# Kernel optimization log

Measured on AMD Instinct MI355X. Metric: run time of the kernel, lower is better.

The kernel has to match this reference:

```python
import jax, jax.numpy as jnp
import numpy as np

EMBED = 768
FFN = 3072
HEADS = 12
HEAD_DIM = EMBED // HEADS
B, T = 4, 2048


def _layer_norm(x, g, b, eps=1e-5):
    m = jnp.mean(x, axis=-1, keepdims=True)
    v = jnp.mean((x - m) ** 2, axis=-1, keepdims=True)
    return (x - m) * jax.lax.rsqrt(v + eps) * g + b


def setup_inputs() -> dict:
    key = jax.random.key(0)
    ks = jax.random.split(key, 8)
    s_e = 1.0 / np.sqrt(EMBED)
    s_f = 1.0 / np.sqrt(FFN)
    # weights stored [in, out] (transpose of torch Linear layout)
    return {
        "x": jax.random.normal(ks[0], (B, T, EMBED), dtype=jnp.float32),
        "ln1_g": jnp.ones((EMBED,), jnp.float32),
        "ln1_b": jnp.zeros((EMBED,), jnp.float32),
        "wq": jax.random.uniform(ks[1], (EMBED, EMBED), jnp.float32, -s_e, s_e),
        "bq": jnp.zeros((EMBED,), jnp.float32),
        "wk": jax.random.uniform(ks[2], (EMBED, EMBED), jnp.float32, -s_e, s_e),
        "bk": jnp.zeros((EMBED,), jnp.float32),
        "wv": jax.random.uniform(ks[3], (EMBED, EMBED), jnp.float32, -s_e, s_e),
        "bv": jnp.zeros((EMBED,), jnp.float32),
        "wo": jax.random.uniform(ks[4], (EMBED, EMBED), jnp.float32, -s_e, s_e),
        "bo": jnp.zeros((EMBED,), jnp.float32),
        "ln2_g": jnp.ones((EMBED,), jnp.float32),
        "ln2_b": jnp.zeros((EMBED,), jnp.float32),
        "w1": jax.random.uniform(ks[5], (EMBED, FFN), jnp.float32, -s_e, s_e),
        "b1": jnp.zeros((FFN,), jnp.float32),
        "w2": jax.random.uniform(ks[6], (FFN, EMBED), jnp.float32, -s_f, s_f),
        "b2": jnp.zeros((EMBED,), jnp.float32),
    }


def reference(x, ln1_g, ln1_b, wq, bq, wk, bk, wv, bv, wo, bo,
              ln2_g, ln2_b, w1, b1, w2, b2):
    Bx, Tx, C = x.shape
    # --- self-attention block (pre-norm) ---
    residual = x
    h = _layer_norm(x, ln1_g, ln1_b)
    q = (h @ wq + bq).reshape(Bx, Tx, HEADS, HEAD_DIM)
    k = (h @ wk + bk).reshape(Bx, Tx, HEADS, HEAD_DIM)
    v = (h @ wv + bv).reshape(Bx, Tx, HEADS, HEAD_DIM)
    scale = 1.0 / np.sqrt(HEAD_DIM)
    attn = jnp.einsum('bqhd,bkhd->bhqk', q, k) * scale  # [B,H,T,T]
    attn = jax.nn.softmax(attn, axis=-1)
    o = jnp.einsum('bhqk,bkhd->bqhd', attn, v).reshape(Bx, Tx, C)
    x = residual + (o @ wo + bo)
    # --- FFN block (pre-norm) ---
    residual = x
    h = _layer_norm(x, ln2_g, ln2_b)
    h = jax.nn.gelu(h @ w1 + b1, approximate=False)
    x = residual + (h @ w2 + b2)
    return x
```

## Files before the change

kernel.cpp:

```cpp
#include <hip/hip_runtime.h>
#include <hip/hip_bf16.h>

#define EMBED 768
#define FFNDIM 3072
#define HEADS 12
#define HDIM  64
#define BB    4
#define TT    2048
#define MTOK  (BB*TT)

typedef __hip_bfloat16 bf16;
typedef __attribute__((ext_vector_type(8))) short short8;
typedef __attribute__((ext_vector_type(4))) float f32x4;
typedef __attribute__((ext_vector_type(16))) float f32x16;
typedef __attribute__((ext_vector_type(4))) unsigned short ushort4v;

__device__ __forceinline__ f32x4 mfma16(short8 a, short8 b, f32x4 c) {
  return __builtin_amdgcn_mfma_f32_16x16x32_bf16(a, b, c, 0, 0, 0);
}
__device__ __forceinline__ f32x16 mfma32(short8 a, short8 b, f32x16 c) {
  return __builtin_amdgcn_mfma_f32_32x32x16_bf16(a, b, c, 0, 0, 0);
}

__device__ __forceinline__ unsigned short f2bf(float f) {
  union { float f; unsigned int u; } v; v.f = f;
  unsigned int u = v.u;
  return (unsigned short)((u + 0x7fffu + ((u >> 16) & 1u)) >> 16);
}

__device__ __forceinline__ unsigned cvtpk(float lo, float hi) {
  unsigned r;
  asm("v_cvt_pk_bf16_f32 %0, %1, %2" : "=v"(r) : "v"(lo), "v"(hi));
  return r;
}
__device__ __forceinline__ void pl32swap(unsigned& vdst, unsigned& vsrc) {
  asm("v_permlane32_swap_b32 %0, %1" : "+v"(vdst), "+v"(vsrc));
}

__device__ __forceinline__ void gl_lds16(const void* g, void* l) {
  __builtin_amdgcn_global_load_lds((const __attribute__((address_space(1))) void*)g,
                                   (__attribute__((address_space(3))) void*)l, 16, 0, 0);
}

struct TArgs {
  const float* src[6];
  bf16* dst[6];
  int K[6];
  int N[6];
};

__global__ __launch_bounds__(256) void transpose_k(TArgs ta) {
  const int mi = blockIdx.z;
  const int K = ta.K[mi], N = ta.N[mi];
  const int nt = N / 32;
  const int bx = blockIdx.x % nt, by = blockIdx.x / nt;
  const int n0 = bx * 32, k0 = by * 32;
  if (k0 >= K) return;
  __shared__ float t[32][33];
  const float* __restrict__ W = ta.src[mi];
  bf16* __restrict__ Wt = ta.dst[mi];
  const int tx = threadIdx.x & 31, ty = threadIdx.x >> 5;
#pragma unroll
  for (int i = 0; i < 4; ++i) {
    int kk = ty + i * 8;
    t[tx][kk] = W[(size_t)(k0 + kk) * N + n0 + tx];
  }
  __syncthreads();
#pragma unroll
  for (int i = 0; i < 4; ++i) {
    int nn = ty + i * 8;
    Wt[(size_t)(n0 + nn) * K + k0 + tx] = __float2bfloat16(t[nn][tx]);
  }
}

__global__ __launch_bounds__(256) void ln_k(const float* __restrict__ x,
                                            const float* __restrict__ g,
                                            const float* __restrict__ b,
                                            bf16* __restrict__ out) {
  const int row = blockIdx.x * 4 + (threadIdx.x >> 6);
  const int lane = threadIdx.x & 63;
  const float* xr = x + (size_t)row * EMBED;
  float4 v[3];
  float s = 0.f;
#pragma unroll
  for (int i = 0; i < 3; ++i) {
    v[i] = *(const float4*)&xr[i * 256 + lane * 4];
    s += v[i].x + v[i].y + v[i].z + v[i].w;
  }
#pragma unroll
  for (int m = 1; m < 64; m <<= 1) s += __shfl_xor(s, m);
  const float mean = s * (1.f / 768.f);
  float ss = 0.f;
#pragma unroll
  for (int i = 0; i < 3; ++i) {
    float dx = v[i].x - mean, dy = v[i].y - mean, dz = v[i].z - mean, dw = v[i].w - mean;
    ss += dx * dx + dy * dy + dz * dz + dw * dw;
  }
#pragma unroll
  for (int m = 1; m < 64; m <<= 1) ss += __shfl_xor(ss, m);
  const float rstd = rsqrtf(ss * (1.f / 768.f) + 1e-5f);
#pragma unroll
  for (int i = 0; i < 3; ++i) {
    float4 g4 = *(const float4*)&g[i * 256 + lane * 4];
    float4 b4 = *(const float4*)&b[i * 256 + lane * 4];
    ushort4v o4;
    o4[0] = f2bf((v[i].x - mean) * rstd * g4.x + b4.x);
    o4[1] = f2bf((v[i].y - mean) * rstd * g4.y + b4.y);
    o4[2] = f2bf((v[i].z - mean) * rstd * g4.z + b4.z);
    o4[3] = f2bf((v[i].w - mean) * rstd * g4.w + b4.w);
    *(ushort4v*)&out[(size_t)row * EMBED + i * 256 + lane * 4] = o4;
  }
}

template <int EPI>
__global__ __launch_bounds__(256) void gemm_bt_k(
    const bf16* __restrict__ A, const bf16* __restrict__ Bt,
    const float* __restrict__ bias, const float* __restrict__ bias2,
    const float* __restrict__ bias3, const float* __restrict__ resid,
    float* __restrict__ outf, bf16* __restrict__ outb,
    bf16* __restrict__ outk, bf16* __restrict__ outvt,
    int N, int K) {
  const int tid = threadIdx.x;
  const int lane = tid & 63;
  const int w = tid >> 6;
  const int wr = w >> 1, wc = w & 1;
  const int l16 = lane & 15, g = lane >> 4;

  const int nbx = N >> 7;
  const int logical = ((int)blockIdx.x & 7) * ((int)gridDim.x >> 3) + ((int)blockIdx.x >> 3);
  const int m0 = (logical / nbx) * 128, n0 = (logical % nbx) * 128;

  __shared__ bf16 Al[2][128 * 32];
  __shared__ bf16 Bl[2][128 * 32];

  f32x4 acc[4][4];
#pragma unroll
  for (int i = 0; i < 4; ++i)
#pragma unroll
    for (int j = 0; j < 4; ++j) acc[i][j] = {0.f, 0.f, 0.f, 0.f};

  const int st_r = lane >> 2;
  const int st_c = ((lane & 3) ^ ((lane >> 3) & 3)) * 8;
  const size_t a_base = (size_t)(m0 + w * 32) * K;
  const size_t b_base = (size_t)(n0 + w * 32) * K;

  auto stage = [&](int bufi, int kt) {
#pragma unroll
    for (int p = 0; p < 2; ++p) {
      gl_lds16(A + a_base + (size_t)(p * 16 + st_r) * K + kt + st_c,
               &Al[bufi][(w * 32 + p * 16) * 32]);
      gl_lds16(Bt + b_base + (size_t)(p * 16 + st_r) * K + kt + st_c,
               &Bl[bufi][(w * 32 + p * 16) * 32]);
    }
  };

  stage(0, 0);
  __syncthreads();
  int buf = 0;
  const int nt = K >> 5;
  const int sw = (l16 >> 1) & 3;
  for (int t = 0; t < nt; ++t) {
    if (t + 1 < nt) stage(buf ^ 1, (t + 1) * 32);
    short8 af[4], bfr[4];
#pragma unroll
    for (int i = 0; i < 4; ++i)
      af[i] = *(const short8*)&Al[buf][(wr * 64 + i * 16 + l16) * 32 + (g ^ sw) * 8];
#pragma unroll
    for (int j = 0; j < 4; ++j)
      bfr[j] = *(const short8*)&Bl[buf][(wc * 64 + j * 16 + l16) * 32 + (g ^ sw) * 8];
#pragma unroll
    for (int i = 0; i < 4; ++i)
#pragma unroll
      for (int j = 0; j < 4; ++j) acc[i][j] = mfma16(af[i], bfr[j], acc[i][j]);
    __syncthreads();
    buf ^= 1;
  }

  const int crow = m0 + wr * 64 + g * 4;
  const int ccol = n0 + wc * 64 + l16;

  if constexpr (EPI == 0) {
    const int region = n0 / EMBED;
    const float* bp = (region == 0) ? bias : (region == 1) ? bias2 : bias3;
    if (region < 2) {
      const float sc = (region == 0) ? 0.125f : 1.0f;
      bf16* __restrict__ dst = (region == 0) ? outb : outk;
#pragma unroll
      for (int j = 0; j < 4; ++j) {
        const int cn = ccol - region * EMBED + j * 16;
        const float bvv = bp[cn];
#pragma unroll
        for (int i = 0; i < 4; ++i)
#pragma unroll
          for (int rr = 0; rr < 4; ++rr) {
            const int m = crow + i * 16 + rr;
            dst[(size_t)m * EMBED + cn] = __float2bfloat16((acc[i][j][rr] + bvv) * sc);
          }
      }
    } else {
#pragma unroll
      for (int j = 0; j < 4; ++j) {
        const int cn = ccol - 2 * EMBED + j * 16;
        const float bvv = bp[cn];
        const int hh = cn >> 6, dd = cn & 63;
#pragma unroll
        for (int i = 0; i < 4; ++i) {
          const int m = crow + i * 16;
          const int bb2 = m >> 11, t = m & 2047;
          ushort4v pk;
#pragma unroll
          for (int rr = 0; rr < 4; ++rr) pk[rr] = f2bf(acc[i][j][rr] + bvv);
          *(ushort4v*)&outvt[((size_t)((bb2 * HEADS + hh) * HDIM + dd)) * TT + t] = pk;
        }
      }
    }
  } else if constexpr (EPI == 1) {
#pragma unroll
    for (int j = 0; j < 4; ++j) {
      const int cn = ccol + j * 16;
      const float bvv = bias[cn];
#pragma unroll
      for (int i = 0; i < 4; ++i)
#pragma unroll
        for (int rr = 0; rr < 4; ++rr) {
          const int m = crow + i * 16 + rr;
          const size_t idx = (size_t)m * N + cn;
          outf[idx] = resid[idx] + acc[i][j][rr] + bvv;
        }
    }
  } else {
#pragma unroll
    for (int j = 0; j < 4; ++j) {
      const int cn = ccol + j * 16;
      const float bvv = bias[cn];
#pragma unroll
      for (int i = 0; i < 4; ++i)
#pragma unroll
        for (int rr = 0; rr < 4; ++rr) {
          const int m = crow + i * 16 + rr;
          const float v = acc[i][j][rr] + bvv;
          const float ge = 0.5f * v * (1.f + erff(v * 0.70710678118f));
          outb[(size_t)m * N + cn] = __float2bfloat16(ge);
        }
    }
  }
}

__global__ __launch_bounds__(256) void flash4_k(const bf16* __restrict__ q,
                                                const bf16* __restrict__ k,
                                                const bf16* __restrict__ vt,
                                                bf16* __restrict__ o) {
  const int tid = threadIdx.x, lane = tid & 63;
  const int l32 = lane & 31, hl = lane >> 5;
  const int w = tid >> 6;
  const int logical = ((int)blockIdx.x & 7) * 96 + ((int)blockIdx.x >> 3);
  const int qt = logical & 15;
  const int hb = logical >> 4;
  const int h = hb % HEADS, b = hb / HEADS;
  const int q0 = (qt * 4 + w) * 32;

  __shared__ bf16 Kl[2][64 * 64];
  __shared__ bf16 Vl[2][64 * 64];

  short8 qf[4];
  {
    const bf16* qp = q + (size_t)(b * TT + q0 + l32) * EMBED + h * HDIM + hl * 8;
#pragma unroll
    for (int c = 0; c < 4; ++c) qf[c] = *(const short8*)&qp[c * 16];
  }

  const bf16* __restrict__ kgs = k + (size_t)(b * TT) * EMBED + h * HDIM;
  const bf16* __restrict__ vgs = vt + ((size_t)((b * HEADS + h) * HDIM)) * TT;

  f32x16 oacc0, oacc1;
#pragma unroll
  for (int i = 0; i < 16; ++i) { oacc0[i] = 0.f; oacc1[i] = 0.f; }
  float mrun = -1.0e30f, lrun = 0.f;

  const int st_rw = w * 8 + (lane >> 3);
  const int st_cs0 = lane & 7;
  auto stage = [&](int buf, int kv) {
#pragma unroll
    for (int p = 0; p < 2; ++p) {
      const int r = p * 32 + st_rw;
      const int cs = st_cs0 ^ (r & 7);
      char* kdst = (char*)&Kl[buf][0] + p * 4096 + w * 1024;
      char* vdst = (char*)&Vl[buf][0] + p * 4096 + w * 1024;
      gl_lds16(kgs + (size_t)(kv + r) * EMBED + cs * 8, kdst);
      gl_lds16(vgs + (size_t)r * TT + kv + cs * 8, vdst);
    }
  };

  auto subtile = [&](int buf, int s2) {
    const int krow = s2 * 32 + l32;
    const char* Kb = (const char*)&Kl[buf][0];
    const char* Vb = (const char*)&Vl[buf][0];
    short8 kf[4];
#pragma unroll
    for (int c = 0; c < 4; ++c)
      kf[c] = *(const short8*)(Kb + krow * 128 + (((2 * c + hl) ^ (krow & 7)) * 16));

    f32x16 s;
#pragma unroll
    for (int i = 0; i < 16; ++i) s[i] = 0.f;
    __builtin_amdgcn_s_setprio(1);
#pragma unroll
    for (int c = 0; c < 4; ++c) s = mfma32(kf[c], qf[c], s);
    __builtin_amdgcn_s_setprio(0);

    short8 vf[4];
#pragma unroll
    for (int ks = 0; ks < 2; ++ks)
#pragma unroll
      for (int dc = 0; dc < 2; ++dc) {
        const int vrow = dc * 32 + l32;
        vf[ks * 2 + dc] = *(const short8*)(
            Vb + vrow * 128 + (((s2 * 4 + ks * 2 + hl) ^ (vrow & 7)) * 16));
      }

    float t8[8];
#pragma unroll
    for (int i = 0; i < 8; ++i) t8[i] = fmaxf(s[2 * i], s[2 * i + 1]);
    float t4a = fmaxf(t8[0], t8[1]), t4b = fmaxf(t8[2], t8[3]);
    float t4c = fmaxf(t8[4], t8[5]), t4d = fmaxf(t8[6], t8[7]);
    float mx = fmaxf(fmaxf(t4a, t4b), fmaxf(t4c, t4d));
    mx = fmaxf(mx, __shfl_xor(mx, 32));

    if (!__all(mx <= mrun + 8.f)) {
      const float mn = fmaxf(mrun, mx);
      const float al = __expf(mrun - mn);
      lrun *= al;
#pragma unroll
      for (int i = 0; i < 16; ++i) { oacc0[i] *= al; oacc1[i] *= al; }
      mrun = mn;
    }

    float p[16];
#pragma unroll
    for (int i = 0; i < 16; ++i) p[i] = __expf(s[i] - mrun);
    float a8[8];
#pragma unroll
    for (int i = 0; i < 8; ++i) a8[i] = p[2 * i] + p[2 * i + 1];
    float ps = ((a8[0] + a8[1]) + (a8[2] + a8[3])) + ((a8[4] + a8[5]) + (a8[6] + a8[7]));
    ps += __shfl_xor(ps, 32);
    lrun += ps;

    union { unsigned u[4]; short8 s8; } pa0, pa1;
    {
      unsigned U = cvtpk(p[0], p[1]), V = cvtpk(p[4], p[5]);
      pl32swap(V, U); pa0.u[0] = U; pa0.u[2] = V;
      unsigned U1 = cvtpk(p[2], p[3]), V1 = cvtpk(p[6], p[7]);
      pl32swap(V1, U1); pa0.u[1] = U1; pa0.u[3] = V1;
    }
    {
      unsigned U = cvtpk(p[8], p[9]), V = cvtpk(p[12], p[13]);
      pl32swap(V, U); pa1.u[0] = U; pa1.u[2] = V;
      unsigned U1 = cvtpk(p[10], p[11]), V1 = cvtpk(p[14], p[15]);
      pl32swap(V1, U1); pa1.u[1] = U1; pa1.u[3] = V1;
    }

    __builtin_amdgcn_s_setprio(1);
    oacc0 = mfma32(vf[0], pa0.s8, oacc0);
    oacc0 = mfma32(vf[2], pa1.s8, oacc0);
    oacc1 = mfma32(vf[1], pa0.s8, oacc1);
    oacc1 = mfma32(vf[3], pa1.s8, oacc1);
    __builtin_amdgcn_s_setprio(0);
  };

  stage(0, 0);
  __syncthreads();
  int buf = 0;
  const int NT = TT / 64;
  for (int t = 0; t < NT; ++t) {
    if (t + 1 < NT) stage(buf ^ 1, (t + 1) * 64);
    subtile(buf, 0);
    subtile(buf, 1);
    __syncthreads();
    buf ^= 1;
  }

  const float inv = 1.f / lrun;
  bf16* op = o + (size_t)(b * TT + q0 + l32) * EMBED + h * HDIM;
#pragma unroll
  for (int a = 0; a < 4; ++a) {
    ushort4v pk4;
#pragma unroll
    for (int bb = 0; bb < 4; ++bb) pk4[bb] = f2bf(oacc0[a * 4 + bb] * inv);
    *(ushort4v*)&op[a * 8 + hl * 4] = pk4;
#pragma unroll
    for (int bb = 0; bb < 4; ++bb) pk4[bb] = f2bf(oacc1[a * 4 + bb] * inv);
    *(ushort4v*)&op[32 + a * 8 + hl * 4] = pk4;
  }
}

extern "C" void kernel_launch(void* const* d_in, const int* in_sizes, int n_in,
                              void* d_out, int out_size, void* d_ws,
                              size_t ws_size, hipStream_t stream) {
  const float* x = (const float*)d_in[0];
  const float* ln1g = (const float*)d_in[1];
  const float* ln1b = (const float*)d_in[2];
  const float* wq = (const float*)d_in[3];
  const float* bq = (const float*)d_in[4];
  const float* wk = (const float*)d_in[5];
  const float* bk = (const float*)d_in[6];
  const float* wv = (const float*)d_in[7];
  const float* bv = (const float*)d_in[8];
  const float* wo = (const float*)d_in[9];
  const float* bo = (const float*)d_in[10];
  const float* ln2g = (const float*)d_in[11];
  const float* ln2b = (const float*)d_in[12];
  const float* w1 = (const float*)d_in[13];
  const float* b1 = (const float*)d_in[14];
  const float* w2 = (const float*)d_in[15];
  const float* b2 = (const float*)d_in[16];
  float* out = (float*)d_out;

  char* ws = (char*)d_ws;
  size_t off = 0;
  auto alloc = [&](size_t bytes) {
    char* p = ws + off;
    off += (bytes + 255) & ~(size_t)255;
    return p;
  };
  bf16* wqkv_t = (bf16*)alloc((size_t)2304 * 768 * 2);
  bf16* wo_t = (bf16*)alloc((size_t)768 * 768 * 2);
  bf16* w1_t = (bf16*)alloc((size_t)3072 * 768 * 2);
  bf16* w2_t = (bf16*)alloc((size_t)768 * 3072 * 2);
  bf16* h = (bf16*)alloc((size_t)MTOK * EMBED * 2);
  char* qkvo = alloc((size_t)MTOK * EMBED * 2 * 4);
  bf16* qb = (bf16*)qkvo;
  bf16* kb = qb + (size_t)MTOK * EMBED;
  bf16* vtb = kb + (size_t)MTOK * EMBED;
  bf16* ob = vtb + (size_t)MTOK * EMBED;
  bf16* h1 = (bf16*)qkvo;
  float* x1 = (float*)alloc((size_t)MTOK * EMBED * 4);
  (void)ws_size;

  TArgs ta;
  ta.src[0] = wq; ta.dst[0] = wqkv_t;                  ta.K[0] = 768;  ta.N[0] = 768;
  ta.src[1] = wk; ta.dst[1] = wqkv_t + 768 * 768;      ta.K[1] = 768;  ta.N[1] = 768;
  ta.src[2] = wv; ta.dst[2] = wqkv_t + 2 * 768 * 768;  ta.K[2] = 768;  ta.N[2] = 768;
  ta.src[3] = wo; ta.dst[3] = wo_t;                    ta.K[3] = 768;  ta.N[3] = 768;
  ta.src[4] = w1; ta.dst[4] = w1_t;                    ta.K[4] = 768;  ta.N[4] = 3072;
  ta.src[5] = w2; ta.dst[5] = w2_t;                    ta.K[5] = 3072; ta.N[5] = 768;

  transpose_k<<<dim3(2304, 1, 6), dim3(256), 0, stream>>>(ta);
  ln_k<<<dim3(MTOK / 4), dim3(256), 0, stream>>>(x, ln1g, ln1b, h);
  gemm_bt_k<0><<<dim3((2304 / 128) * (MTOK / 128)), dim3(256), 0, stream>>>(
      h, wqkv_t, bq, bk, bv, nullptr, nullptr, qb, kb, vtb, 2304, 768);
  flash4_k<<<dim3(16 * HEADS * BB), dim3(256), 0, stream>>>(qb, kb, vtb, ob);
  gemm_bt_k<1><<<dim3((768 / 128) * (MTOK / 128)), dim3(256), 0, stream>>>(
      ob, wo_t, bo, nullptr, nullptr, x, x1, nullptr, nullptr, nullptr, 768, 768);
  ln_k<<<dim3(MTOK / 4), dim3(256), 0, stream>>>(x1, ln2g, ln2b, h);
  gemm_bt_k<2><<<dim3((3072 / 128) * (MTOK / 128)), dim3(256), 0, stream>>>(
      h, w1_t, b1, nullptr, nullptr, nullptr, nullptr, h1, nullptr, nullptr, 3072, 768);
  gemm_bt_k<1><<<dim3((768 / 128) * (MTOK / 128)), dim3(256), 0, stream>>>(
      h1, w2_t, b2, nullptr, nullptr, x1, out, nullptr, nullptr, nullptr, 768, 3072);
}
```

Baseline: 320.2 us.

## Use 128x64 GEMM tiles for N=768 projections and exp2-based softmax

```diff
diff --git a/kernel.cpp b/kernel.cpp
--- a/kernel.cpp
+++ b/kernel.cpp
@@ -28,6 +28,14 @@
   return (unsigned short)((u + 0x7fffu + ((u >> 16) & 1u)) >> 16);
 }
 
+__device__ __forceinline__ float fexp2(float x) {
+#if __has_builtin(__builtin_amdgcn_exp2f)
+  return __builtin_amdgcn_exp2f(x);
+#else
+  return exp2f(x);
+#endif
+}
+
 __device__ __forceinline__ unsigned cvtpk(float lo, float hi) {
   unsigned r;
   asm("v_cvt_pk_bf16_f32 %0, %1, %2" : "=v"(r) : "v"(lo), "v"(hi));
@@ -41,6 +49,9 @@
   __builtin_amdgcn_global_load_lds((const __attribute__((address_space(1))) void*)g,
                                    (__attribute__((address_space(3))) void*)l, 16, 0, 0);
 }
+
+#define QSCALE 0.18033688011112042f
+#define DEFER_THR 11.54f
 
 struct TArgs {
   const float* src[6];
@@ -112,7 +123,7 @@
   }
 }
 
-template <int EPI>
+template <int EPI, int TN>
 __global__ __launch_bounds__(256) void gemm_bt_k(
     const bf16* __restrict__ A, const bf16* __restrict__ Bt,
     const float* __restrict__ bias, const float* __restrict__ bias2,
@@ -120,37 +131,45 @@
     float* __restrict__ outf, bf16* __restrict__ outb,
     bf16* __restrict__ outk, bf16* __restrict__ outvt,
     int N, int K) {
+  constexpr int MI = (TN == 128) ? 4 : 2;
   const int tid = threadIdx.x;
   const int lane = tid & 63;
   const int w = tid >> 6;
-  const int wr = w >> 1, wc = w & 1;
   const int l16 = lane & 15, g = lane >> 4;
-
-  const int nbx = N >> 7;
+  const int wrbase = (TN == 128) ? (w >> 1) * 64 : w * 32;
+  const int wcbase = (TN == 128) ? (w & 1) * 64 : 0;
+
+  const int nbx = N / TN;
   const int logical = ((int)blockIdx.x & 7) * ((int)gridDim.x >> 3) + ((int)blockIdx.x >> 3);
-  const int m0 = (logical / nbx) * 128, n0 = (logical % nbx) * 128;
+  const int m0 = (logical / nbx) * 128, n0 = (logical % nbx) * TN;
 
   __shared__ bf16 Al[2][128 * 32];
-  __shared__ bf16 Bl[2][128 * 32];
-
-  f32x4 acc[4][4];
-#pragma unroll
-  for (int i = 0; i < 4; ++i)
+  __shared__ bf16 Bl[2][TN * 32];
+
+  f32x4 acc[MI][4];
+#pragma unroll
+  for (int i = 0; i < MI; ++i)
 #pragma unroll
     for (int j = 0; j < 4; ++j) acc[i][j] = {0.f, 0.f, 0.f, 0.f};
 
   const int st_r = lane >> 2;
   const int st_c = ((lane & 3) ^ ((lane >> 3) & 3)) * 8;
   const size_t a_base = (size_t)(m0 + w * 32) * K;
-  const size_t b_base = (size_t)(n0 + w * 32) * K;
+  const size_t b_base = (TN == 128) ? (size_t)(n0 + w * 32) * K
+                                    : (size_t)(n0 + w * 16) * K;
 
   auto stage = [&](int bufi, int kt) {
 #pragma unroll
-    for (int p = 0; p < 2; ++p) {
+    for (int p = 0; p < 2; ++p)
       gl_lds16(A + a_base + (size_t)(p * 16 + st_r) * K + kt + st_c,
                &Al[bufi][(w * 32 + p * 16) * 32]);
-      gl_lds16(Bt + b_base + (size_t)(p * 16 + st_r) * K + kt + st_c,
-               &Bl[bufi][(w * 32 + p * 16) * 32]);
+    if constexpr (TN == 128) {
+#pragma unroll
+      for (int p = 0; p < 2; ++p)
+        gl_lds16(Bt + b_base + (size_t)(p * 16 + st_r) * K + kt + st_c,
+                 &Bl[bufi][(w * 32 + p * 16) * 32]);
+    } else {
+      gl_lds16(Bt + b_base + (size_t)st_r * K + kt + st_c, &Bl[bufi][(w * 16) * 32]);
     }
   };
 
@@ -161,36 +180,36 @@
   const int sw = (l16 >> 1) & 3;
   for (int t = 0; t < nt; ++t) {
     if (t + 1 < nt) stage(buf ^ 1, (t + 1) * 32);
-    short8 af[4], bfr[4];
-#pragma unroll
-    for (int i = 0; i < 4; ++i)
-      af[i] = *(const short8*)&Al[buf][(wr * 64 + i * 16 + l16) * 32 + (g ^ sw) * 8];
+    short8 af[MI], bfr[4];
+#pragma unroll
+    for (int i = 0; i < MI; ++i)
+      af[i] = *(const short8*)&Al[buf][(wrbase + i * 16 + l16) * 32 + (g ^ sw) * 8];
 #pragma unroll
     for (int j = 0; j < 4; ++j)
-      bfr[j] = *(const short8*)&Bl[buf][(wc * 64 + j * 16 + l16) * 32 + (g ^ sw) * 8];
-#pragma unroll
-    for (int i = 0; i < 4; ++i)
+      bfr[j] = *(const short8*)&Bl[buf][(wcbase + j * 16 + l16) * 32 + (g ^ sw) * 8];
+#pragma unroll
+    for (int i = 0; i < MI; ++i)
 #pragma unroll
       for (int j = 0; j < 4; ++j) acc[i][j] = mfma16(af[i], bfr[j], acc[i][j]);
     __syncthreads();
     buf ^= 1;
   }
 
-  const int crow = m0 + wr * 64 + g * 4;
-  const int ccol = n0 + wc * 64 + l16;
+  const int crow = m0 + wrbase + g * 4;
+  const int ccol = n0 + wcbase + l16;
 
   if constexpr (EPI == 0) {
     const int region = n0 / EMBED;
     const float* bp = (region == 0) ? bias : (region == 1) ? bias2 : bias3;
     if (region < 2) {
-      const float sc = (region == 0) ? 0.125f : 1.0f;
+      const float sc = (region == 0) ? QSCALE : 1.0f;
       bf16* __restrict__ dst = (region == 0) ? outb : outk;
 #pragma unroll
       for (int j = 0; j < 4; ++j) {
         const int cn = ccol - region * EMBED + j * 16;
         const float bvv = bp[cn];
 #pragma unroll
-        for (int i = 0; i < 4; ++i)
+        for (int i = 0; i < MI; ++i)
 #pragma unroll
           for (int rr = 0; rr < 4; ++rr) {
             const int m = crow + i * 16 + rr;
@@ -204,7 +223,7 @@
         const float bvv = bp[cn];
         const int hh = cn >> 6, dd = cn & 63;
 #pragma unroll
-        for (int i = 0; i < 4; ++i) {
+        for (int i = 0; i < MI; ++i) {
           const int m = crow + i * 16;
           const int bb2 = m >> 11, t = m & 2047;
           ushort4v pk;
@@ -220,7 +239,7 @@
       const int cn = ccol + j * 16;
       const float bvv = bias[cn];
 #pragma unroll
-      for (int i = 0; i < 4; ++i)
+      for (int i = 0; i < MI; ++i)
 #pragma unroll
         for (int rr = 0; rr < 4; ++rr) {
           const int m = crow + i * 16 + rr;
@@ -234,7 +253,7 @@
       const int cn = ccol + j * 16;
       const float bvv = bias[cn];
 #pragma unroll
-      for (int i = 0; i < 4; ++i)
+      for (int i = 0; i < MI; ++i)
 #pragma unroll
         for (int rr = 0; rr < 4; ++rr) {
           const int m = crow + i * 16 + rr;
@@ -246,7 +265,7 @@
   }
 }
 
-__global__ __launch_bounds__(256) void flash4_k(const bf16* __restrict__ q,
+__global__ __launch_bounds__(256) void flash5_k(const bf16* __restrict__ q,
                                                 const bf16* __restrict__ k,
                                                 const bf16* __restrict__ vt,
                                                 bf16* __restrict__ o) {
@@ -318,17 +337,17 @@
             Vb + vrow * 128 + (((s2 * 4 + ks * 2 + hl) ^ (vrow & 7)) * 16));
       }
 
-    float t8[8];
-#pragma unroll
-    for (int i = 0; i < 8; ++i) t8[i] = fmaxf(s[2 * i], s[2 * i + 1]);
-    float t4a = fmaxf(t8[0], t8[1]), t4b = fmaxf(t8[2], t8[3]);
-    float t4c = fmaxf(t8[4], t8[5]), t4d = fmaxf(t8[6], t8[7]);
-    float mx = fmaxf(fmaxf(t4a, t4b), fmaxf(t4c, t4d));
+    float m0 = fmaxf(fmaxf(s[0], s[1]), s[2]);
+    float m1 = fmaxf(fmaxf(s[3], s[4]), s[5]);
+    float m2 = fmaxf(fmaxf(s[6], s[7]), s[8]);
+    float m3 = fmaxf(fmaxf(s[9], s[10]), s[11]);
+    float m4 = fmaxf(fmaxf(s[12], s[13]), s[14]);
+    float mx = fmaxf(fmaxf(fmaxf(m0, m1), fmaxf(m2, m3)), fmaxf(m4, s[15]));
     mx = fmaxf(mx, __shfl_xor(mx, 32));
 
-    if (!__all(mx <= mrun + 8.f)) {
+    if (!__all(mx <= mrun + DEFER_THR)) {
       const float mn = fmaxf(mrun, mx);
-      const float al = __expf(mrun - mn);
+      const float al = fexp2(mrun - mn);
       lrun *= al;
 #pragma unroll
       for (int i = 0; i < 16; ++i) { oacc0[i] *= al; oacc1[i] *= al; }
@@ -337,7 +356,7 @@
 
     float p[16];
 #pragma unroll
-    for (int i = 0; i < 16; ++i) p[i] = __expf(s[i] - mrun);
+    for (int i = 0; i < 16; ++i) p[i] = fexp2(s[i] - mrun);
     float a8[8];
 #pragma unroll
     for (int i = 0; i < 8; ++i) a8[i] = p[2 * i] + p[2 * i + 1];
@@ -446,14 +465,14 @@
 
   transpose_k<<<dim3(2304, 1, 6), dim3(256), 0, stream>>>(ta);
   ln_k<<<dim3(MTOK / 4), dim3(256), 0, stream>>>(x, ln1g, ln1b, h);
-  gemm_bt_k<0><<<dim3((2304 / 128) * (MTOK / 128)), dim3(256), 0, stream>>>(
+  gemm_bt_k<0, 128><<<dim3((2304 / 128) * (MTOK / 128)), dim3(256), 0, stream>>>(
       h, wqkv_t, bq, bk, bv, nullptr, nullptr, qb, kb, vtb, 2304, 768);
-  flash4_k<<<dim3(16 * HEADS * BB), dim3(256), 0, stream>>>(qb, kb, vtb, ob);
-  gemm_bt_k<1><<<dim3((768 / 128) * (MTOK / 128)), dim3(256), 0, stream>>>(
+  flash5_k<<<dim3(16 * HEADS * BB), dim3(256), 0, stream>>>(qb, kb, vtb, ob);
+  gemm_bt_k<1, 64><<<dim3((768 / 64) * (MTOK / 128)), dim3(256), 0, stream>>>(
       ob, wo_t, bo, nullptr, nullptr, x, x1, nullptr, nullptr, nullptr, 768, 768);
   ln_k<<<dim3(MTOK / 4), dim3(256), 0, stream>>>(x1, ln2g, ln2b, h);
-  gemm_bt_k<2><<<dim3((3072 / 128) * (MTOK / 128)), dim3(256), 0, stream>>>(
+  gemm_bt_k<2, 128><<<dim3((3072 / 128) * (MTOK / 128)), dim3(256), 0, stream>>>(
       h, w1_t, b1, nullptr, nullptr, nullptr, nullptr, h1, nullptr, nullptr, 3072, 768);
-  gemm_bt_k<1><<<dim3((768 / 128) * (MTOK / 128)), dim3(256), 0, stream>>>(
+  gemm_bt_k<1, 64><<<dim3((768 / 64) * (MTOK / 128)), dim3(256), 0, stream>>>(
       h1, w2_t, b2, nullptr, nullptr, x1, out, nullptr, nullptr, nullptr, 768, 3072);
 }
```

Result: no change. 317.1 us (-1.0%).
